# Kernel optimization log

Hardware: AMD Instinct MI355X
Metric: run time of the kernel (lower is better)

## Reference

```python
import jax, jax.numpy as jnp
import numpy as np
from jax import lax

K = 31          # mip_kernel
P_LO, P_HI = 0.01, 0.99
ALPHA = 0.15
MU = 10.0
PD_ITERS = 30
TAU = 0.125
SIG = 0.125
THETA = 1.0
EPS = 1e-6


def _max_pool(x, k):
    # torch F.max_pool2d with stride=1, padding=k//2 pads with -inf
    p = k // 2
    return lax.reduce_window(
        x, -jnp.inf, lax.max,
        window_dimensions=(1, 1, k, k),
        window_strides=(1, 1, 1, 1),
        padding=[(0, 0), (0, 0), (p, p), (p, p)])


def _forward_grad(u):
    # forward differences, zero-padded on the far edge (same shape as u)
    dx = jnp.pad(u[..., :, 1:] - u[..., :, :-1], ((0, 0), (0, 0), (0, 0), (0, 1)))
    dy = jnp.pad(u[..., 1:, :] - u[..., :-1, :], ((0, 0), (0, 0), (0, 1), (0, 0)))
    return dx, dy


def _divergence(px, py):
    div_x = px - jnp.pad(px[..., :, :-1], ((0, 0), (0, 0), (0, 0), (1, 0)))
    div_y = py - jnp.pad(py[..., :-1, :], ((0, 0), (0, 0), (1, 0), (0, 0)))
    return div_x + div_y


def _robust_normalize(x):
    B = x.shape[0]
    flat = x.reshape(B, -1)
    lo = jnp.quantile(flat, P_LO, axis=1).reshape(B, 1, 1, 1)
    hi = jnp.quantile(flat, P_HI, axis=1).reshape(B, 1, 1, 1)
    return jnp.clip((x - lo) / (hi - lo + EPS), 0.0, 1.0)


def setup_inputs() -> dict:
    key = jax.random.key(0)
    Iy = jax.random.uniform(key, (16, 3, 512, 512), dtype=jnp.float32)
    return {"Iy": Iy}


def reference(Iy):
    B = Iy.shape[0]
    R, G, Bc = Iy[:, 0:1], Iy[:, 1:2], Iy[:, 2:3]

    Rmax = _max_pool(R, K)
    GBmax = jnp.maximum(_max_pool(G, K), _max_pool(Bc, K))
    Dmip_abs = jnp.abs(Rmax - GBmax)

    N_hat = _robust_normalize(Dmip_abs + R)

    dxh, dyh = _forward_grad(N_hat)
    grad_mag = jnp.sqrt(dxh * dxh + dyh * dyh + EPS)
    # sigma_mode == 'median' -> per-image median of grad magnitude
    sigma = jnp.quantile(grad_mag.reshape(B, -1), 0.5, axis=1).reshape(B, 1, 1, 1)
    sigma = jnp.maximum(sigma, EPS)

    Wx = 1.0 + MU * jnp.exp(-jnp.abs(dxh) / sigma)
    Wy = 1.0 + MU * jnp.exp(-jnp.abs(dyh) / sigma)

    def step(carry, _):
        u, u_bar, px, py = carry
        dx, dy = _forward_grad(u_bar)
        px = jnp.clip(px + SIG * dx, -ALPHA * Wx, ALPHA * Wx)
        py = jnp.clip(py + SIG * dy, -ALPHA * Wy, ALPHA * Wy)
        div_p = _divergence(px, py)
        v = u + TAU * div_p
        u_new = (v + TAU * N_hat) / (1.0 + TAU)
        u_bar = u_new + THETA * (u_new - u)
        return (u_new, u_bar, px, py), None

    z = jnp.zeros_like(N_hat)
    (u, _, _, _), _ = lax.scan(step, (N_hat, N_hat, z, z), None, length=PD_ITERS)
    return jnp.clip(u, 0.0, 1.0)
```

## Files before the change

kernel.cpp:

```cpp
#include <hip/hip_runtime.h>
#include <hip/hip_bf16.h>
#include <hip/hip_fp16.h>
#include <math.h>

#define NPIX   262144
#define NP     4194304
#define NBINS  8192
#define HSUB   16
#define RB     8
#define SIG    0.125f
#define TAUC   0.125f
#define ALPHAC 0.15f
#define MUC    10.0f
#define EPSC   1e-6f
#define NEGINF -3.4e38f
#define IVT    (1.0f / (1.0f + TAUC))

__device__ __forceinline__ void cvt8h(float4 raw, float* d) {
    const __half2* h = (const __half2*)&raw;
#pragma unroll
    for (int j = 0; j < 4; ++j) {
        float2 f = __half22float2(h[j]);
        d[2 * j] = f.x; d[2 * j + 1] = f.y;
    }
}
__device__ __forceinline__ void ld8h(const __half* p, float* d) {
    cvt8h(*(const float4*)p, d);
}
__device__ __forceinline__ float4 pk8h(const float* s) {
    float4 r; __half2* h = (__half2*)&r;
#pragma unroll
    for (int j = 0; j < 4; ++j) h[j] = __floats2half2_rn(s[2 * j], s[2 * j + 1]);
    return r;
}
__device__ __forceinline__ float bnd(float d, float inv) {
    return ALPHAC * (1.f + MUC * __expf(-fabsf(d) * inv));
}
__device__ __forceinline__ float clmp(float v, float b) {
    return fminf(fmaxf(v, -b), b);
}


__global__ __launch_bounds__(512) void hpass3_k(const float* __restrict__ Iy,
                                                __half* __restrict__ H) {
    __shared__ float rowbuf[8][512];
    __shared__ float PB[8][512];
    __shared__ float SB[8][512];
    int tid = threadIdx.x;
    int plane = blockIdx.y;
    int y0 = blockIdx.x * 8;

#pragma unroll
    for (int q = 0; q < 2; ++q) {
        int idx = q * 512 + tid;
        int r = idx >> 7;
        int x4 = (idx & 127) << 2;
        float4 v;
        if (plane < 16) {
            v = *(const float4*)(Iy + (size_t)(plane * 3) * NPIX + (size_t)(y0 + r) * 512 + x4);
        } else {
            int b = plane - 16;
            float4 g = *(const float4*)(Iy + ((size_t)(b * 3) + 1) * NPIX + (size_t)(y0 + r) * 512 + x4);
            float4 bb = *(const float4*)(Iy + ((size_t)(b * 3) + 2) * NPIX + (size_t)(y0 + r) * 512 + x4);
            v = make_float4(fmaxf(g.x, bb.x), fmaxf(g.y, bb.y), fmaxf(g.z, bb.z), fmaxf(g.w, bb.w));
        }
        *(float4*)(&rowbuf[r][x4]) = v;
    }
    __syncthreads();

    if (tid < 272) {
        int type = tid / 136;
        int rem = tid % 136;
        int r = rem / 17;
        int seg = rem % 17;
        int s0 = seg * 31;
        if (type == 0) {
            float run = rowbuf[r][s0];
            PB[r][s0] = run;
            for (int j = 1; j < 31; ++j) {
                int idx = s0 + j;
                if (idx < 512) { run = fmaxf(run, rowbuf[r][idx]); PB[r][idx] = run; }
            }
        } else {
            int s1 = min(s0 + 30, 511);
            float run = rowbuf[r][s1];
            SB[r][s1] = run;
            for (int j = s1 - 1; j >= s0; --j) { run = fmaxf(run, rowbuf[r][j]); SB[r][j] = run; }
        }
    }
    __syncthreads();

    int x = tid, a = x - 15, bc = x + 15;
#pragma unroll
    for (int r = 0; r < 8; ++r) {
        float o;
        if (a < 0)        o = PB[r][bc];
        else if (bc > 511) o = fmaxf(SB[r][a], PB[r][511]);
        else              o = fmaxf(SB[r][a], PB[r][bc]);
        H[(size_t)plane * NPIX + (size_t)(y0 + r) * 512 + x] = __float2half_rn(o);
    }
}

__global__ __launch_bounds__(64) void vpass2h_k(const __half* __restrict__ H,
                                                __half* __restrict__ V) {
    int x = blockIdx.x * 64 + threadIdx.x;
    int s = blockIdx.y;
    const __half* in = H + (size_t)blockIdx.z * NPIX;
    __half*      out = V + (size_t)blockIdx.z * NPIX;
    int s0 = s * 31;

    float Sprev[31];
    if (s > 0) {
        int p0 = s0 - 31;
        float v[31];
#pragma unroll
        for (int j = 0; j < 31; ++j) v[j] = __half2float(in[(size_t)(p0 + j) * 512 + x]);
        float acc = NEGINF;
#pragma unroll
        for (int j = 30; j >= 0; --j) { acc = fmaxf(acc, v[j]); Sprev[j] = acc; }
    } else {
#pragma unroll
        for (int j = 0; j < 31; ++j) Sprev[j] = NEGINF;
    }

    float P = NEGINF;
#pragma unroll
    for (int r = 0; r < 31; ++r) {
        float vv = (s0 + r < 512) ? __half2float(in[(size_t)(s0 + r) * 512 + x]) : NEGINF;
        P = fmaxf(P, vv);
        int i = s0 + r - 15;
        if (i >= 0 && i <= 511) {
            int a = s0 + r - 30;
            float o;
            if (a < 0)       o = P;
            else if (r == 30) o = P;
            else              o = fmaxf(Sprev[r + 1], P);
            out[(size_t)i * 512 + x] = __float2half_rn(o);
        }
    }
}

__global__ __launch_bounds__(256) void combineh_k(const __half* __restrict__ V,
                                                  const float* __restrict__ Iy,
                                                  __half* __restrict__ xb) {
    size_t i = ((size_t)blockIdx.x * 256 + threadIdx.x) * 8;
    int b = (int)(i >> 18);
    size_t off = i & (NPIX - 1);
    float vr[8], vm[8];
    ld8h(V + (size_t)b * NPIX + off, vr);
    ld8h(V + (size_t)(16 + b) * NPIX + off, vm);
    const float* R = Iy + (size_t)(b * 3) * NPIX + off;
    float4 r0 = *(const float4*)R;
    float4 r1 = *(const float4*)(R + 4);
    float rr[8] = {r0.x, r0.y, r0.z, r0.w, r1.x, r1.y, r1.z, r1.w};
    float a[8];
#pragma unroll
    for (int j = 0; j < 8; ++j) a[j] = fabsf(vr[j] - vm[j]) + rr[j];
    *(float4*)(xb + i) = pk8h(a);
}


__global__ __launch_bounds__(1024) void hist2_k(const __half* __restrict__ v,
                                                int* __restrict__ hist) {
    __shared__ int lh[NBINS];
    int s = blockIdx.x, b = blockIdx.y, tid = threadIdx.x;
    for (int i = tid; i < NBINS; i += 1024) lh[i] = 0;
    __syncthreads();
    const __half* p = v + (size_t)b * NPIX + (size_t)s * (NPIX / HSUB);
    for (int i = tid; i < NPIX / HSUB; i += 1024) {
        int bin = (int)(__half2float(p[i]) * (NBINS * 0.5f));
        bin = min(max(bin, 0), NBINS - 1);
        atomicAdd(&lh[bin], 1);
    }
    __syncthreads();
    for (int i = tid; i < NBINS; i += 1024) {
        int c = lh[i];
        if (c) atomicAdd(&hist[b * NBINS + i], c);
    }
}

__global__ __launch_bounds__(1024) void gradhisth_k(const __half* __restrict__ nh,
                                                    int* __restrict__ hist) {
    __shared__ int lh[NBINS];
    int s = blockIdx.x, b = blockIdx.y, tid = threadIdx.x;
    for (int i = tid; i < NBINS; i += 1024) lh[i] = 0;
    __syncthreads();
    const __half* p = nh + (size_t)b * NPIX;
    int base = s * (NPIX / HSUB);
    for (int ii = tid; ii < NPIX / HSUB; ii += 1024) {
        int i = base + ii;
        float c = __half2float(p[i]);
        int x = i & 511, y = i >> 9;
        float dx = (x < 511) ? __half2float(p[i + 1])   - c : 0.f;
        float dy = (y < 511) ? __half2float(p[i + 512]) - c : 0.f;
        float gm = sqrtf(dx * dx + dy * dy + EPSC);
        int bin = (int)(gm * (NBINS * 0.5f));
        bin = min(max(bin, 0), NBINS - 1);
        atomicAdd(&lh[bin], 1);
    }
    __syncthreads();
    for (int i = tid; i < NBINS; i += 1024) {
        int c = lh[i];
        if (c) atomicAdd(&hist[b * NBINS + i], c);
    }
}

__global__ __launch_bounds__(1024) void quant2_k(const int* __restrict__ hist,
                                                 float* __restrict__ scal,
                                                 float q0, float q1, int s0, int s1) {
    __shared__ int csum[1025];
    __shared__ int wsum[16];
    int b = blockIdx.x, tid = threadIdx.x;
    const int* h = hist + b * NBINS;
    int s = 0;
#pragma unroll
    for (int j = 0; j < NBINS / 1024; ++j) s += h[tid * (NBINS / 1024) + j];

    int lane = tid & 63, wave = tid >> 6;
    int v = s;
#pragma unroll
    for (int off = 1; off < 64; off <<= 1) {
        int n = __shfl_up(v, off, 64);
        if (lane >= off) v += n;
    }
    if (lane == 63) wsum[wave] = v;
    __syncthreads();
    if (wave == 0 && lane < 16) {
        int w = wsum[lane];
#pragma unroll
        for (int off = 1; off < 16; off <<= 1) {
            int n = __shfl_up(w, off, 64);
            if (lane >= off) w += n;
        }
        wsum[lane] = w;
    }
    __syncthreads();
    int incl = v + (wave > 0 ? wsum[wave - 1] : 0);
    csum[tid + 1] = incl;
    if (tid == 0) csum[0] = 0;
    __syncthreads();

#pragma unroll
    for (int pass = 0; pass < 2; ++pass) {
        int slot = pass ? s1 : s0;
        if (slot < 0) continue;
        float q = pass ? q1 : q0;
        float t = q * (float)(NPIX - 1);
        if ((float)csum[tid] <= t && (float)csum[tid + 1] > t) {
            const int per = NBINS / 1024;
            int cb = csum[tid];
            int bin = tid * per;
            int hv = 1;
            for (int j = 0; j < per; ++j) {
                hv = h[tid * per + j];
                if ((float)(cb + hv) > t) { bin = tid * per + j; break; }
                cb += hv;
            }
            float k = t - (float)cb;
            scal[b * 4 + slot] = ((float)bin + (k + 0.5f) / (float)hv) * (2.0f / NBINS);
        }
    }
}

__global__ __launch_bounds__(256) void nhat2h_k(const __half* __restrict__ xb,
                                                const float* __restrict__ scal,
                                                __half* __restrict__ nhh) {
    size_t i = ((size_t)blockIdx.x * 256 + threadIdx.x) * 8;
    int b = (int)(i >> 18);
    float lo = scal[b * 4 + 0], hi = scal[b * 4 + 1];
    float inv = 1.0f / (hi - lo + EPSC);
    float v[8]; ld8h(xb + i, v);
    float a[8];
#pragma unroll
    for (int j = 0; j < 8; ++j)
        a[j] = fminf(fmaxf((v[j] - lo) * inv, 0.f), 1.f);
    *(float4*)(nhh + i) = pk8h(a);
}

__global__ __launch_bounds__(256) void pdf2_k(const __half* __restrict__ u,
                                              const __half* __restrict__ up,
                                              const __half* __restrict__ pxO,
                                              const __half* __restrict__ pyO,
                                              __half* __restrict__ pxN,
                                              __half* __restrict__ pyN,
                                              const __half* __restrict__ nh,
                                              const float* __restrict__ scal,
                                              __half* __restrict__ u1g,
                                              __half* __restrict__ u2g,
                                              float* __restrict__ outF,
                                              int last) {
    __shared__ __align__(16) char smem[76800];
    __half (*ubar0h)[512] = (__half(*)[512])smem;
    __half (*py2l)[512]   = (__half(*)[512])smem;
    __half (*u0l)[512]    = (__half(*)[512])(smem + 12288);
    __half (*nhl)[512]    = (__half(*)[512])(smem + 24576);
    __half (*px1)[512]    = (__half(*)[512])(smem + 36864);
    __half (*py1)[512]    = (__half(*)[512])(smem + 47104);
    __half (*u1l)[512]    = (__half(*)[512])(smem + 58368);
    __half (*px2l)[512]   = (__half(*)[512])(smem + 68608);

    int tid = threadIdx.x;
    int sub = tid >> 6, lane = tid & 63, x0 = lane * 8;
    int y0 = blockIdx.x * RB;
    int b = blockIdx.y;
    size_t plane = (size_t)b * NPIX;
    float sgm = fmaxf(scal[b * 4 + 2], EPSC);
    float inv = 1.0f / sgm;
    const float4 z4 = make_float4(0.f, 0.f, 0.f, 0.f);

    for (int i = sub; i < 12; i += 4) {
        int g = y0 - 2 + i;
        if (g >= 0 && g < 512) {
            size_t off = plane + (size_t)g * 512 + x0;
            float4 uraw = *(const float4*)(u + off);
            float uu[8], pp[8], ub[8];
            cvt8h(uraw, uu); ld8h(up + off, pp);
#pragma unroll
            for (int j = 0; j < 8; ++j) ub[j] = 2.f * uu[j] - pp[j];
            *(float4*)&ubar0h[i][x0] = pk8h(ub);
            *(float4*)&u0l[i][x0] = uraw;
            *(float4*)&nhl[i][x0] = *(const float4*)(nh + off);
        } else {
            *(float4*)&ubar0h[i][x0] = z4;
            *(float4*)&u0l[i][x0] = z4;
            *(float4*)&nhl[i][x0] = z4;
        }
    }
    __syncthreads();

    for (int c = sub; c < 11; c += 4) {
        int g = y0 - 2 + c;
        if (g >= 0 && g < 512) {
            size_t off = plane + (size_t)g * 512 + x0;
            float nhc[8], nhd[8], ubc[8], ubd[8];
            ld8h(&nhl[c][x0], nhc);
            ld8h(&nhl[c + 1][x0], nhd);
            ld8h(&ubar0h[c][x0], ubc);
            ld8h(&ubar0h[c + 1][x0], ubd);
            float nhRr = (lane < 63) ? __half2float(nhl[c][x0 + 8]) : 0.f;
            float ubRr = (lane < 63) ? __half2float(ubar0h[c][x0 + 8]) : 0.f;
            bool rD = (g < 511);
            float py0v[8]; ld8h(pyO + off, py0v);
            float pyv[8];
#pragma unroll
            for (int j = 0; j < 8; ++j) {
                float by = bnd(rD ? (nhd[j] - nhc[j]) : 0.f, inv);
                float dy = rD ? (ubd[j] - ubc[j]) : 0.f;
                pyv[j] = clmp(py0v[j] + SIG * dy, by);
            }
            *(float4*)&py1[c][x0] = pk8h(pyv);
            if (c >= 1) {
                float px0v[8]; ld8h(pxO + off, px0v);
                float pxv[8];
#pragma unroll
                for (int j = 0; j < 8; ++j) {
                    int x = x0 + j;
                    bool xok = (x < 511);
                    float nhr = (j < 7) ? nhc[j + 1] : nhRr;
                    float ubr = (j < 7) ? ubc[j + 1] : ubRr;
                    float bx = bnd(xok ? (nhr - nhc[j]) : 0.f, inv);
                    float dx = xok ? (ubr - ubc[j]) : 0.f;
                    pxv[j] = clmp(px0v[j] + SIG * dx, bx);
                }
                *(float4*)&px1[c - 1][x0] = pk8h(pxv);
            }
        } else {
            *(float4*)&py1[c][x0] = z4;
            if (c >= 1) *(float4*)&px1[c - 1][x0] = z4;
        }
    }
    __syncthreads();

    for (int a = sub; a < 10; a += 4) {
        int g = y0 - 1 + a;
        if (g >= 0 && g < 512) {
            float u0v[8]; ld8h(&u0l[a + 1][x0], u0v);
            float nhc[8];  ld8h(&nhl[a + 1][x0], nhc);
            float px1c[8]; ld8h(&px1[a][x0], px1c);
            float py1c[8]; ld8h(&py1[a + 1][x0], py1c);
            float py1u[8]; ld8h(&py1[a][x0], py1u);
            float pxl = (x0 > 0) ? __half2float(px1[a][x0 - 1]) : 0.f;
            bool gU = (g > 0);
            float uv[8];
#pragma unroll
            for (int j = 0; j < 8; ++j) {
                int x = x0 + j;
                float left = (x > 0) ? ((j > 0) ? px1c[j - 1] : pxl) : 0.f;
                float div = px1c[j] - left + py1c[j] - (gU ? py1u[j] : 0.f);
                uv[j] = (u0v[j] + TAUC * div + TAUC * nhc[j]) * IVT;
            }
            float4 packed = pk8h(uv);
            *(float4*)&u1l[a][x0] = packed;
            if (!last && g >= y0 && g < y0 + RB) {
                size_t off = plane + (size_t)g * 512 + x0;
                *(float4*)(u1g + off) = packed;
            }
        } else {
            *(float4*)&u1l[a][x0] = z4;
        }
    }
    __syncthreads();

    for (int e = sub; e < 9; e += 4) {
        int g = y0 - 1 + e;
        if (g >= 0) {
            size_t off = plane + (size_t)g * 512 + x0;
            float u1c[8], u0c[8], u1d[8], u0d[8];
            ld8h(&u1l[e][x0], u1c);     ld8h(&u0l[e + 1][x0], u0c);
            ld8h(&u1l[e + 1][x0], u1d); ld8h(&u0l[e + 2][x0], u0d);
            float nhc[8], nhd[8];
            ld8h(&nhl[e + 1][x0], nhc); ld8h(&nhl[e + 2][x0], nhd);
            float ubc[8], ubd[8];
#pragma unroll
            for (int j = 0; j < 8; ++j) {
                ubc[j] = 2.f * u1c[j] - u0c[j];
                ubd[j] = 2.f * u1d[j] - u0d[j];
            }
            float ubRr = (lane < 63) ? (2.f * __half2float(u1l[e][x0 + 8]) - __half2float(u0l[e + 1][x0 + 8])) : 0.f;
            float nhRr = (lane < 63) ? __half2float(nhl[e + 1][x0 + 8]) : 0.f;
            bool rD = (g < 511);
            float py1c[8]; ld8h(&py1[e + 1][x0], py1c);
            float pyv[8];
#pragma unroll
            for (int j = 0; j < 8; ++j) {
                float by = bnd(rD ? (nhd[j] - nhc[j]) : 0.f, inv);
                float dy = rD ? (ubd[j] - ubc[j]) : 0.f;
                pyv[j] = clmp(py1c[j] + SIG * dy, by);
            }
            float4 pyp = pk8h(pyv);
            *(float4*)&py2l[e][x0] = pyp;
            if (!last && g >= y0) *(float4*)(pyN + off) = pyp;
            if (e >= 1) {
                float px1c[8]; ld8h(&px1[e][x0], px1c);
                float pxv[8];
#pragma unroll
                for (int j = 0; j < 8; ++j) {
                    int x = x0 + j;
                    bool xok = (x < 511);
                    float nhr = (j < 7) ? nhc[j + 1] : nhRr;
                    float ubr = (j < 7) ? ubc[j + 1] : ubRr;
                    float bx = bnd(xok ? (nhr - nhc[j]) : 0.f, inv);
                    float dx = xok ? (ubr - ubc[j]) : 0.f;
                    pxv[j] = clmp(px1c[j] + SIG * dx, bx);
                }
                float4 pxp = pk8h(pxv);
                *(float4*)&px2l[e - 1][x0] = pxp;
                if (!last) *(float4*)(pxN + off) = pxp;
            }
        } else {
            *(float4*)&py2l[e][x0] = z4;
        }
    }
    __syncthreads();

    for (int d = sub; d < 8; d += 4) {
        int g = y0 + d;
        size_t off = plane + (size_t)g * 512 + x0;
        float px2c[8]; ld8h(&px2l[d][x0], px2c);
        float py2c[8]; ld8h(&py2l[d + 1][x0], py2c);
        float py2u[8]; ld8h(&py2l[d][x0], py2u);
        float pxl = (x0 > 0) ? __half2float(px2l[d][x0 - 1]) : 0.f;
        float u1c[8]; ld8h(&u1l[d + 1][x0], u1c);
        float nhc[8]; ld8h(&nhl[d + 2][x0], nhc);
        bool gU = (g > 0);
        float uv[8];
#pragma unroll
        for (int j = 0; j < 8; ++j) {
            int x = x0 + j;
            float left = (x > 0) ? ((j > 0) ? px2c[j - 1] : pxl) : 0.f;
            float div = px2c[j] - left + py2c[j] - (gU ? py2u[j] : 0.f);
            uv[j] = (u1c[j] + TAUC * div + TAUC * nhc[j]) * IVT;
        }
        if (last) {
            float4 o0, o1;
            o0.x = fminf(fmaxf(uv[0], 0.f), 1.f);
            o0.y = fminf(fmaxf(uv[1], 0.f), 1.f);
            o0.z = fminf(fmaxf(uv[2], 0.f), 1.f);
            o0.w = fminf(fmaxf(uv[3], 0.f), 1.f);
            o1.x = fminf(fmaxf(uv[4], 0.f), 1.f);
            o1.y = fminf(fmaxf(uv[5], 0.f), 1.f);
            o1.z = fminf(fmaxf(uv[6], 0.f), 1.f);
            o1.w = fminf(fmaxf(uv[7], 0.f), 1.f);
            *(float4*)(outF + off)     = o0;
            *(float4*)(outF + off + 4) = o1;
        } else {
            *(float4*)(u2g + off) = pk8h(uv);
        }
    }
}

extern "C" void kernel_launch(void* const* d_in, const int* in_sizes, int n_in,
                              void* d_out, int out_size, void* d_ws, size_t ws_size,
                              hipStream_t stream) {
    const float* Iy = (const float*)d_in[0];
    float* out = (float*)d_out;

    dim3 hist_g(HSUB, 16);
    dim3 pd2_g(512 / RB, 16);

    __half* hb  = (__half*)d_ws;
    __half* nhh = hb;
    __half* HA  = hb + (size_t)NP;
    __half* HB  = hb + (size_t)2 * NP;
    __half* HC  = hb + (size_t)3 * NP;
    __half* HD  = hb + (size_t)4 * NP;
    __half* pxA = hb + (size_t)5 * NP;
    __half* pyA = hb + (size_t)6 * NP;
    __half* pxB = hb + (size_t)7 * NP;
    __half* pyB = hb + (size_t)8 * NP;
    __half* xbh = hb + (size_t)9 * NP;
    __half* Hh  = hb + (size_t)10 * NP;
    __half* Vh  = hb + (size_t)1 * NP;
    int*    hist = (int*)(hb + (size_t)12 * NP);
    float*  scal = (float*)(hist + 16 * NBINS);

    hpass3_k<<<dim3(64, 32), dim3(512), 0, stream>>>(Iy, Hh);
    vpass2h_k<<<dim3(8, 17, 32), dim3(64), 0, stream>>>(Hh, Vh);
    combineh_k<<<NP / 2048, 256, 0, stream>>>(Vh, Iy, xbh);

    hipMemsetAsync(hist, 0, 16 * NBINS * sizeof(int), stream);
    hist2_k<<<hist_g, 1024, 0, stream>>>(xbh, hist);
    quant2_k<<<16, 1024, 0, stream>>>(hist, scal, 0.01f, 0.99f, 0, 1);
    nhat2h_k<<<NP / 2048, 256, 0, stream>>>(xbh, scal, nhh);

    hipMemsetAsync(hist, 0, 16 * NBINS * sizeof(int), stream);
    gradhisth_k<<<hist_g, 1024, 0, stream>>>(nhh, hist);
    quant2_k<<<16, 1024, 0, stream>>>(hist, scal, 0.5f, 0.5f, 2, -1);
    hipMemsetAsync(pxA, 0, (size_t)2 * NP * sizeof(__half), stream);

    const __half* ucur = nhh;
    const __half* uprev = nhh;
    __half* pxs[2] = {pxA, pxB};
    __half* pys[2] = {pyA, pyB};
    for (int k = 0; k < 15; ++k) {
        int cur = k & 1;
        __half* u1o = (k & 1) ? HC : HA;
        __half* u2o = (k & 1) ? HD : HB;
        pdf2_k<<<pd2_g, 256, 0, stream>>>(ucur, uprev,
                                          pxs[cur], pys[cur],
                                          pxs[cur ^ 1], pys[cur ^ 1],
                                          nhh, scal, u1o, u2o, out,
                                          (k == 14) ? 1 : 0);
        uprev = u1o;
        ucur = u2o;
    }
}
```

Measured before the change: 485.1 us.

## Fuse second dual update into final primal stage, recompute upper py row

Merges the second dual (px/py) update stage into the final primal update stage of the two-iteration fused kernel. Each thread recomputes the py row above from shared memory, and gets the left px neighbour through a wavefront shuffle instead of staging it in LDS. This removes one barrier and two shared buffers, shrinking LDS from 76.8KB to about 56KB. That may let more blocks fit per CU, at the cost of some redundant bound/exp arithmetic, with fp16 rounding mimicked via rth.

```diff
diff --git a/kernel.cpp b/kernel.cpp
--- a/kernel.cpp
+++ b/kernel.cpp
@@ -38,6 +38,9 @@
 }
 __device__ __forceinline__ float clmp(float v, float b) {
     return fminf(fmaxf(v, -b), b);
+}
+__device__ __forceinline__ float rth(float v) {
+    return __half2float(__float2half_rn(v));
 }
 
 
@@ -289,15 +292,13 @@
                                               __half* __restrict__ u2g,
                                               float* __restrict__ outF,
                                               int last) {
-    __shared__ __align__(16) char smem[76800];
+    __shared__ __align__(16) char smem[56320];
     __half (*ubar0h)[512] = (__half(*)[512])smem;
-    __half (*py2l)[512]   = (__half(*)[512])smem;
+    __half (*u1l)[512]    = (__half(*)[512])smem;
     __half (*u0l)[512]    = (__half(*)[512])(smem + 12288);
-    __half (*nhl)[512]    = (__half(*)[512])(smem + 24576);
-    __half (*px1)[512]    = (__half(*)[512])(smem + 36864);
-    __half (*py1)[512]    = (__half(*)[512])(smem + 47104);
-    __half (*u1l)[512]    = (__half(*)[512])(smem + 58368);
-    __half (*px2l)[512]   = (__half(*)[512])(smem + 68608);
+    __half (*nhl)[512]    = (__half(*)[512])(smem + 22528);
+    __half (*px1)[512]    = (__half(*)[512])(smem + 34816);
+    __half (*py1)[512]    = (__half(*)[512])(smem + 45056);
 
     int tid = threadIdx.x;
     int sub = tid >> 6, lane = tid & 63, x0 = lane * 8;
@@ -318,11 +319,11 @@
 #pragma unroll
             for (int j = 0; j < 8; ++j) ub[j] = 2.f * uu[j] - pp[j];
             *(float4*)&ubar0h[i][x0] = pk8h(ub);
-            *(float4*)&u0l[i][x0] = uraw;
+            if (i >= 1 && i <= 10) *(float4*)&u0l[i - 1][x0] = uraw;
             *(float4*)&nhl[i][x0] = *(const float4*)(nh + off);
         } else {
             *(float4*)&ubar0h[i][x0] = z4;
-            *(float4*)&u0l[i][x0] = z4;
+            if (i >= 1 && i <= 10) *(float4*)&u0l[i - 1][x0] = z4;
             *(float4*)&nhl[i][x0] = z4;
         }
     }
@@ -374,7 +375,7 @@
     for (int a = sub; a < 10; a += 4) {
         int g = y0 - 1 + a;
         if (g >= 0 && g < 512) {
-            float u0v[8]; ld8h(&u0l[a + 1][x0], u0v);
+            float u0v[8]; ld8h(&u0l[a][x0], u0v);
             float nhc[8];  ld8h(&nhl[a + 1][x0], nhc);
             float px1c[8]; ld8h(&px1[a][x0], px1c);
             float py1c[8]; ld8h(&py1[a + 1][x0], py1c);
@@ -401,74 +402,71 @@
     }
     __syncthreads();
 
-    for (int e = sub; e < 9; e += 4) {
-        int g = y0 - 1 + e;
-        if (g >= 0) {
-            size_t off = plane + (size_t)g * 512 + x0;
-            float u1c[8], u0c[8], u1d[8], u0d[8];
-            ld8h(&u1l[e][x0], u1c);     ld8h(&u0l[e + 1][x0], u0c);
-            ld8h(&u1l[e + 1][x0], u1d); ld8h(&u0l[e + 2][x0], u0d);
-            float nhc[8], nhd[8];
-            ld8h(&nhl[e + 1][x0], nhc); ld8h(&nhl[e + 2][x0], nhd);
-            float ubc[8], ubd[8];
-#pragma unroll
-            for (int j = 0; j < 8; ++j) {
-                ubc[j] = 2.f * u1c[j] - u0c[j];
-                ubd[j] = 2.f * u1d[j] - u0d[j];
-            }
-            float ubRr = (lane < 63) ? (2.f * __half2float(u1l[e][x0 + 8]) - __half2float(u0l[e + 1][x0 + 8])) : 0.f;
-            float nhRr = (lane < 63) ? __half2float(nhl[e + 1][x0 + 8]) : 0.f;
-            bool rD = (g < 511);
-            float py1c[8]; ld8h(&py1[e + 1][x0], py1c);
-            float pyv[8];
-#pragma unroll
-            for (int j = 0; j < 8; ++j) {
-                float by = bnd(rD ? (nhd[j] - nhc[j]) : 0.f, inv);
-                float dy = rD ? (ubd[j] - ubc[j]) : 0.f;
-                pyv[j] = clmp(py1c[j] + SIG * dy, by);
-            }
-            float4 pyp = pk8h(pyv);
-            *(float4*)&py2l[e][x0] = pyp;
-            if (!last && g >= y0) *(float4*)(pyN + off) = pyp;
-            if (e >= 1) {
-                float px1c[8]; ld8h(&px1[e][x0], px1c);
-                float pxv[8];
-#pragma unroll
-                for (int j = 0; j < 8; ++j) {
-                    int x = x0 + j;
-                    bool xok = (x < 511);
-                    float nhr = (j < 7) ? nhc[j + 1] : nhRr;
-                    float ubr = (j < 7) ? ubc[j + 1] : ubRr;
-                    float bx = bnd(xok ? (nhr - nhc[j]) : 0.f, inv);
-                    float dx = xok ? (ubr - ubc[j]) : 0.f;
-                    pxv[j] = clmp(px1c[j] + SIG * dx, bx);
-                }
-                float4 pxp = pk8h(pxv);
-                *(float4*)&px2l[e - 1][x0] = pxp;
-                if (!last) *(float4*)(pxN + off) = pxp;
-            }
-        } else {
-            *(float4*)&py2l[e][x0] = z4;
-        }
-    }
-    __syncthreads();
-
     for (int d = sub; d < 8; d += 4) {
         int g = y0 + d;
         size_t off = plane + (size_t)g * 512 + x0;
-        float px2c[8]; ld8h(&px2l[d][x0], px2c);
-        float py2c[8]; ld8h(&py2l[d + 1][x0], py2c);
-        float py2u[8]; ld8h(&py2l[d][x0], py2u);
-        float pxl = (x0 > 0) ? __half2float(px2l[d][x0 - 1]) : 0.f;
-        float u1c[8]; ld8h(&u1l[d + 1][x0], u1c);
-        float nhc[8]; ld8h(&nhl[d + 2][x0], nhc);
-        bool gU = (g > 0);
-        float uv[8];
+        bool gU = (g > 0), rD = (g < 511);
+
+        float u1m[8], u1c[8], u1d_[8], u0m[8], u0c[8], u0d_[8];
+        ld8h(&u1l[d][x0],     u1m);  ld8h(&u0l[d][x0],     u0m);
+        ld8h(&u1l[d + 1][x0], u1c);  ld8h(&u0l[d + 1][x0], u0c);
+        ld8h(&u1l[d + 2][x0], u1d_); ld8h(&u0l[d + 2][x0], u0d_);
+        float nhm[8], nhc[8], nhd[8];
+        ld8h(&nhl[d + 1][x0], nhm);
+        ld8h(&nhl[d + 2][x0], nhc);
+        ld8h(&nhl[d + 3][x0], nhd);
+        float ubm[8], ubc[8], ubd[8];
+#pragma unroll
+        for (int j = 0; j < 8; ++j) {
+            ubm[j] = 2.f * u1m[j] - u0m[j];
+            ubc[j] = 2.f * u1c[j] - u0c[j];
+            ubd[j] = 2.f * u1d_[j] - u0d_[j];
+        }
+
+        float py1m[8]; ld8h(&py1[d + 1][x0], py1m);
+        float py2u[8];
+#pragma unroll
+        for (int j = 0; j < 8; ++j) {
+            float by = bnd(nhc[j] - nhm[j], inv);
+            py2u[j] = rth(clmp(py1m[j] + SIG * (ubc[j] - ubm[j]), by));
+        }
+
+        float py1c[8]; ld8h(&py1[d + 2][x0], py1c);
+        float pyv[8];
+#pragma unroll
+        for (int j = 0; j < 8; ++j) {
+            float by = bnd(rD ? (nhd[j] - nhc[j]) : 0.f, inv);
+            float dy = rD ? (ubd[j] - ubc[j]) : 0.f;
+            pyv[j] = rth(clmp(py1c[j] + SIG * dy, by));
+        }
+
+        float px1c[8]; ld8h(&px1[d + 1][x0], px1c);
+        float ubRr = (lane < 63) ? (2.f * __half2float(u1l[d + 1][x0 + 8]) - __half2float(u0l[d + 1][x0 + 8])) : 0.f;
+        float nhRr = (lane < 63) ? __half2float(nhl[d + 2][x0 + 8]) : 0.f;
+        float pxv[8];
 #pragma unroll
         for (int j = 0; j < 8; ++j) {
             int x = x0 + j;
-            float left = (x > 0) ? ((j > 0) ? px2c[j - 1] : pxl) : 0.f;
-            float div = px2c[j] - left + py2c[j] - (gU ? py2u[j] : 0.f);
+            bool xok = (x < 511);
+            float nhr = (j < 7) ? nhc[j + 1] : nhRr;
+            float ubr = (j < 7) ? ubc[j + 1] : ubRr;
+            float bx = bnd(xok ? (nhr - nhc[j]) : 0.f, inv);
+            float dx = xok ? (ubr - ubc[j]) : 0.f;
+            pxv[j] = rth(clmp(px1c[j] + SIG * dx, bx));
+        }
+        float pxl = __shfl_up(pxv[7], 1, 64);
+
+        if (!last) {
+            *(float4*)(pxN + off) = pk8h(pxv);
+            *(float4*)(pyN + off) = pk8h(pyv);
+        }
+
+        float uv[8];
+#pragma unroll
+        for (int j = 0; j < 8; ++j) {
+            int x = x0 + j;
+            float left = (x > 0) ? ((j > 0) ? pxv[j - 1] : pxl) : 0.f;
+            float div = pxv[j] - left + pyv[j] - (gU ? py2u[j] : 0.f);
             uv[j] = (u1c[j] + TAUC * div + TAUC * nhc[j]) * IVT;
         }
         if (last) {
```

After: 497.6 us. 2.6% more time.
